# Kernel optimization log

Hardware: AMD Instinct MI355X
Metric: run time of the kernel (lower is better)

Reference implementation:

```python
import jax, jax.numpy as jnp
import numpy as np

B, T, XD, ZD, H = 1024, 1000, 8, 8, 256


def setup_inputs() -> dict:
    key = jax.random.key(0)
    ks = jax.random.split(key, 10)
    # monotonically increasing time grid, identical per batch element: [B, T, 1]
    t = jnp.broadcast_to(jnp.linspace(0.0, 10.0, T, dtype=jnp.float32)[None, :, None], (B, T, 1))
    x = jax.random.normal(ks[0], (B, T, XD), jnp.float32)
    z = jax.random.normal(ks[1], (B, T, ZD), jnp.float32)
    event_t = jax.random.uniform(ks[2], (B, 1), jnp.float32, 3.0, 7.0)
    z_jump = jax.random.normal(ks[3], (B, ZD), jnp.float32)
    in_dim = 3 * (XD + ZD)

    def lin(k, fan_in, fan_out):
        return jax.random.normal(k, (fan_in, fan_out), jnp.float32) * (1.0 / np.sqrt(fan_in))

    W1 = lin(ks[4], in_dim, H); b1 = jnp.zeros((H,), jnp.float32)
    W2 = lin(ks[5], H, H);     b2 = jnp.zeros((H,), jnp.float32)
    W3 = lin(ks[6], H, H);     b3 = jnp.zeros((H,), jnp.float32)
    W4 = lin(ks[7], H, XD);    b4 = jnp.zeros((XD,), jnp.float32)
    return dict(t=t, x=x, z=z, event_t=event_t, z_jump=z_jump,
                W1=W1, b1=b1, W2=W2, b2=b2, W3=W3, b3=b3, W4=W4, b4=b4)


def reference(t, x, z, event_t, z_jump, W1, b1, W2, b2, W3, b3, W4, b4):
    # all_initial = cat(x[:,0], z[:,0]) : [B, XD+ZD]
    all_initial = jnp.concatenate([x[:, 0], z[:, 0]], axis=-1)

    def de_func(x_cur, z_eff):
        xtzt = jnp.concatenate([x_cur, z_eff], axis=-1)                      # [B, XD+ZD]
        inp = jnp.concatenate([all_initial, xtzt - all_initial, xtzt], -1)   # [B, 3*(XD+ZD)]
        h = jax.nn.elu(inp @ W1 + b1)
        h = jax.nn.elu(h @ W2 + b2)
        h = jax.nn.elu(h @ W3 + b3)
        return h @ W4 + b4                                                   # [B, XD]

    t_seq = jnp.moveaxis(t, 1, 0)   # [T, B, 1]
    z_seq = jnp.moveaxis(z, 1, 0)   # [T, B, ZD]
    dt = t_seq[1:] - t_seq[:-1]     # [T-1, B, 1]

    def step(x_cur, step_in):
        t_i, dt_i, z_i = step_in
        # event: once t passes event_t, exogenous z jumps to z_jump
        z_eff = jnp.where(t_i >= event_t, z_jump, z_i)
        x_next = x_cur + dt_i * de_func(x_cur, z_eff)  # explicit Euler step
        return x_next, x_next

    x0 = x[:, 0]  # initial condition [B, XD]
    _, xs = jax.lax.scan(step, x0, (t_seq[:-1], dt, z_seq[:-1]))
    sol = jnp.concatenate([x0[None], xs], axis=0)  # [T, B, XD]
    return jnp.moveaxis(sol, 0, 1)                 # [B, T, XD]
```

## Files before the change

kernel.cpp:

```cpp
#include <hip/hip_runtime.h>
#include <cstdint>
#include <cstddef>

typedef __bf16 bf16x8 __attribute__((ext_vector_type(8)));
typedef float f32x4 __attribute__((ext_vector_type(4)));

#define HD 256
#define TLEN 1000
#define NSTEP 999

#define W1R_OFF 0
#define W2R_OFF 16384
#define W3R_OFF 81920
#define W4R_OFF 147456
#define WS_ELEMS 151552

__device__ __forceinline__ void wg_barrier() {
  asm volatile("s_waitcnt lgkmcnt(0)\n\ts_barrier" ::: "memory");
}

__global__ void prep_weights(const float* __restrict__ W1, const float* __restrict__ b1,
                             const float* __restrict__ W2, const float* __restrict__ W3,
                             const float* __restrict__ W4, __bf16* __restrict__ ws) {
  int tid = blockIdx.x * blockDim.x + threadIdx.x;
  if (tid >= WS_ELEMS) return;
  float val = 0.0f;
  if (tid < W2R_OFF) {
    int t = tid;
    int j = t & 7, lane = (t >> 3) & 63, tt = (t >> 9) & 1, kb = (t >> 10) & 1, w = (t >> 11) & 7;
    int k = kb * 32 + ((lane >> 4) * 8) + j;
    int n = w * 32 + tt * 16 + (lane & 15);
    if (k < 48) val = W1[k * HD + n];
    else if (k == 48) val = b1[n];
  } else if (tid < W3R_OFF) {
    int t = tid - W2R_OFF;
    int j = t & 7, lane = (t >> 3) & 63, tt = (t >> 9) & 1, kb = (t >> 10) & 7, w = (t >> 13) & 7;
    int k = kb * 32 + ((lane >> 4) * 8) + j;
    int n = w * 32 + tt * 16 + (lane & 15);
    val = W2[k * HD + n];
  } else if (tid < W4R_OFF) {
    int t = tid - W3R_OFF;
    int j = t & 7, lane = (t >> 3) & 63, tt = (t >> 9) & 1, kb = (t >> 10) & 7, w = (t >> 13) & 7;
    int k = kb * 32 + ((lane >> 4) * 8) + j;
    int n = w * 32 + tt * 16 + (lane & 15);
    val = W3[k * HD + n];
  } else {
    int t = tid - W4R_OFF;
    int j = t & 7, lane = (t >> 3) & 63, kb = (t >> 9) & 7;
    int k = kb * 32 + ((lane >> 4) * 8) + j;
    int n = lane & 15;
    val = (n < 8) ? W4[k * 8 + n] : 0.0f;
  }
  ws[tid] = (__bf16)val;
}

__global__ __launch_bounds__(512, 2) void ode_main(
    const float* __restrict__ t_g, const float* __restrict__ x_g,
    const float* __restrict__ z_g, const float* __restrict__ ev_g,
    const float* __restrict__ zj_g, const float* __restrict__ b2_g,
    const float* __restrict__ b3_g, const float* __restrict__ b4_g,
    const __bf16* __restrict__ ws, float* __restrict__ out) {
  __shared__ __align__(16) __bf16 h_a[16 * 264];
  __shared__ __align__(16) __bf16 h_b[16 * 264];
  __shared__ __align__(16) __bf16 w4sh[4096];
  __shared__ __align__(16) float x_cur[16 * 12];
  __shared__ __align__(16) float z_eff[16 * 12];
  __shared__ __align__(16) float x0s[16 * 12];
  __shared__ __align__(16) float z0s[16 * 12];
  __shared__ __align__(16) float zjs[16 * 12];
  __shared__ float evs[16];

  const int tid  = threadIdx.x;
  const int lane = tid & 63;
  const int wid  = tid >> 6;
  const int bcol = lane & 15;
  const int q    = lane >> 4;
  const int b0   = blockIdx.x * 16;

  if (tid < 128) {
    int m = tid >> 3, d = tid & 7;
    size_t gb = (size_t)(b0 + m);
    float x0 = x_g[gb * (TLEN * 8) + d];
    float z0 = z_g[gb * (TLEN * 8) + d];
    x0s[m * 12 + d] = x0;
    z0s[m * 12 + d] = z0;
    x_cur[m * 12 + d] = x0;
    zjs[m * 12 + d] = zj_g[gb * 8 + d];
    out[gb * (TLEN * 8) + d] = x0;
    if (d == 0) evs[m] = ev_g[gb];
  }
  {
    const uint32_t* s4 = (const uint32_t*)(ws + W4R_OFF);
    uint32_t* d4 = (uint32_t*)w4sh;
#pragma unroll
    for (int k = 0; k < 4; ++k) d4[tid * 4 + k] = s4[tid * 4 + k];
  }
  __syncthreads();

  if (tid < 128) {
    int m = tid >> 3, d = tid & 7;
    float t0 = t_g[0];
    z_eff[m * 12 + d] = (t0 >= evs[m]) ? zjs[m * 12 + d] : z0s[m * 12 + d];
  }

  const bf16x8* wsv = (const bf16x8*)ws;
  bf16x8 w1f[2][2], w2f[8][2], w3f[8][2];
#pragma unroll
  for (int kb = 0; kb < 2; ++kb)
#pragma unroll
    for (int tt = 0; tt < 2; ++tt)
      w1f[kb][tt] = wsv[(W1R_OFF / 8) + ((wid * 2 + kb) * 2 + tt) * 64 + lane];
#pragma unroll
  for (int kb = 0; kb < 8; ++kb)
#pragma unroll
    for (int tt = 0; tt < 2; ++tt) {
      w2f[kb][tt] = wsv[(W2R_OFF / 8) + ((wid * 8 + kb) * 2 + tt) * 64 + lane];
      w3f[kb][tt] = wsv[(W3R_OFF / 8) + ((wid * 8 + kb) * 2 + tt) * 64 + lane];
    }

  f32x4 b2v[2], b3v[2];
#pragma unroll
  for (int tt = 0; tt < 2; ++tt) {
    int n0 = wid * 32 + tt * 16 + q * 4;
    b2v[tt] = *(const f32x4*)(b2_g + n0);
    b3v[tt] = *(const f32x4*)(b3_g + n0);
  }
  f32x4 b4v = {0.f, 0.f, 0.f, 0.f};
  if (wid == 0 && q < 2) b4v = *(const f32x4*)(b4_g + q * 4);

  const int m1 = lane >> 2;
  const int d0 = (lane & 3) * 2;
  float2 zjf = make_float2(0.f, 0.f);
  float ev1 = 0.f;
  if (wid == 1) {
    zjf.x = zjs[m1 * 12 + d0];
    zjf.y = zjs[m1 * 12 + d0 + 1];
    ev1 = evs[m1];
  }

  f32x4 sub0, sub1;
  bf16x8 a0c;
  {
    const float* base = ((q & 1) ? z0s : x0s) + bcol * 12;
    f32x4 r0 = *(const f32x4*)(base);
    f32x4 r1 = *(const f32x4*)(base + 4);
    sub0 = r0; sub1 = r1;
#pragma unroll
    for (int e = 0; e < 4; ++e) { a0c[e] = (__bf16)r0[e]; a0c[e + 4] = (__bf16)r1[e]; }
  }
  bf16x8 zf;
#pragma unroll
  for (int e = 0; e < 8; ++e) zf[e] = (__bf16)0.f;
  bf16x8 k48f = zf;
  k48f[0] = (__bf16)1.0f;

  __syncthreads();

  float tc = t_g[0];

  auto layer = [&](const __bf16* src, __bf16* dst, const bf16x8 (*wf)[2], const f32x4* bv) {
    bf16x8 bfr[8];
    const bf16x8* hp = (const bf16x8*)src;
#pragma unroll
    for (int kb = 0; kb < 8; ++kb) bfr[kb] = hp[bcol * 33 + kb * 4 + q];
#pragma unroll
    for (int tt = 0; tt < 2; ++tt) {
      f32x4 c = bv[tt];
#pragma unroll
      for (int kb = 0; kb < 8; ++kb)
        c = __builtin_amdgcn_mfma_f32_16x16x32_bf16(wf[kb][tt], bfr[kb], c, 0, 0, 0);
      union { __bf16 h4[4]; unsigned long long u; } pk;
#pragma unroll
      for (int e = 0; e < 4; ++e) {
        float v = c[e];
        v = (v > 0.f) ? v : (__expf(v) - 1.0f);
        pk.h4[e] = (__bf16)v;
      }
      *(unsigned long long*)(dst + bcol * 264 + wid * 32 + tt * 16 + q * 4) = pk.u;
    }
  };

#pragma unroll 1
  for (int i = 0; i < NSTEP; ++i) {
    float tn = t_g[i + 1];
    float2 zpre = make_float2(0.f, 0.f);
    if (wid == 1)
      zpre = *(const float2*)(z_g + ((size_t)(b0 + m1) * TLEN + (i + 1)) * 8 + d0);

    {
      const float* rp = ((q & 1) ? z_eff : x_cur) + bcol * 12;
      f32x4 r0 = *(const f32x4*)(rp);
      f32x4 r1 = *(const f32x4*)(rp + 4);
      bf16x8 f0, f1;
      if (q < 2) {
        f0 = a0c;
#pragma unroll
        for (int e = 0; e < 4; ++e) { f1[e] = (__bf16)r0[e]; f1[e + 4] = (__bf16)r1[e]; }
      } else {
#pragma unroll
        for (int e = 0; e < 4; ++e) {
          f0[e] = (__bf16)(r0[e] - sub0[e]);
          f0[e + 4] = (__bf16)(r1[e] - sub1[e]);
        }
        f1 = (q == 2) ? k48f : zf;
      }
#pragma unroll
      for (int tt = 0; tt < 2; ++tt) {
        f32x4 c = {0.f, 0.f, 0.f, 0.f};
        c = __builtin_amdgcn_mfma_f32_16x16x32_bf16(w1f[0][tt], f0, c, 0, 0, 0);
        c = __builtin_amdgcn_mfma_f32_16x16x32_bf16(w1f[1][tt], f1, c, 0, 0, 0);
        union { __bf16 h4[4]; unsigned long long u; } pk;
#pragma unroll
        for (int e = 0; e < 4; ++e) {
          float v = c[e];
          v = (v > 0.f) ? v : (__expf(v) - 1.0f);
          pk.h4[e] = (__bf16)v;
        }
        *(unsigned long long*)(h_a + bcol * 264 + wid * 32 + tt * 16 + q * 4) = pk.u;
      }
    }
    wg_barrier();
    layer(h_a, h_b, w2f, b2v);
    wg_barrier();
    layer(h_b, h_a, w3f, b3v);
    wg_barrier();

    float dt = tn - tc;
    if (wid == 0) {
      const bf16x8* hp = (const bf16x8*)h_a;
      const bf16x8* w4p = (const bf16x8*)w4sh;
      f32x4 c = b4v;
#pragma unroll
      for (int kb = 0; kb < 8; ++kb)
        c = __builtin_amdgcn_mfma_f32_16x16x32_bf16(w4p[kb * 64 + lane],
                                                    hp[bcol * 33 + kb * 4 + q], c, 0, 0, 0);
      if (q < 2) {
        f32x4 xc = *(const f32x4*)(x_cur + bcol * 12 + q * 4);
        f32x4 xn;
#pragma unroll
        for (int e = 0; e < 4; ++e) xn[e] = xc[e] + dt * c[e];
        *(f32x4*)(x_cur + bcol * 12 + q * 4) = xn;
        *(f32x4*)(out + ((size_t)(b0 + bcol) * TLEN + (i + 1)) * 8 + q * 4) = xn;
      }
    } else if (wid == 1) {
      bool jmp = (tn >= ev1);
      float2 zev = make_float2(jmp ? zjf.x : zpre.x, jmp ? zjf.y : zpre.y);
      *(float2*)(z_eff + m1 * 12 + d0) = zev;
    }
    tc = tn;
    wg_barrier();
  }
}

extern "C" void kernel_launch(void* const* d_in, const int* in_sizes, int n_in,
                              void* d_out, int out_size, void* d_ws, size_t ws_size,
                              hipStream_t stream) {
  const float* t  = (const float*)d_in[0];
  const float* x  = (const float*)d_in[1];
  const float* z  = (const float*)d_in[2];
  const float* ev = (const float*)d_in[3];
  const float* zj = (const float*)d_in[4];
  const float* W1 = (const float*)d_in[5];
  const float* b1 = (const float*)d_in[6];
  const float* W2 = (const float*)d_in[7];
  const float* b2 = (const float*)d_in[8];
  const float* W3 = (const float*)d_in[9];
  const float* b3 = (const float*)d_in[10];
  const float* W4 = (const float*)d_in[11];
  const float* b4 = (const float*)d_in[12];
  __bf16* ws = (__bf16*)d_ws;
  float* out = (float*)d_out;

  prep_weights<<<592, 256, 0, stream>>>(W1, b1, W2, W3, W4, ws);
  ode_main<<<64, 512, 0, stream>>>(t, x, z, ev, zj, b2, b3, b4, ws, out);
}
```

Measured before the change: 1.833 ms.

## Halve workgroup to 4 waves and split final layer across all waves

Each workgroup now runs 4 waves instead of 8, and each wave holds weight fragments for 64 output columns instead of 32, so each wave issues twice the MFMAs per layer. The last layer, previously done by wave 0 alone from shared memory, is split across all four waves using register-resident W4 fragments. Their partial sums go through shared memory and are reduced by 128 threads before the Euler update. This cuts barrier participants and the serialized single-wave tail, at the cost of doubled register pressure per wave and fewer waves to hide latency.

```diff
diff --git a/kernel.cpp b/kernel.cpp
--- a/kernel.cpp
+++ b/kernel.cpp
@@ -54,7 +54,7 @@
   ws[tid] = (__bf16)val;
 }
 
-__global__ __launch_bounds__(512, 2) void ode_main(
+__global__ __launch_bounds__(256, 1) void ode_main(
     const float* __restrict__ t_g, const float* __restrict__ x_g,
     const float* __restrict__ z_g, const float* __restrict__ ev_g,
     const float* __restrict__ zj_g, const float* __restrict__ b2_g,
@@ -62,7 +62,7 @@
     const __bf16* __restrict__ ws, float* __restrict__ out) {
   __shared__ __align__(16) __bf16 h_a[16 * 264];
   __shared__ __align__(16) __bf16 h_b[16 * 264];
-  __shared__ __align__(16) __bf16 w4sh[4096];
+  __shared__ __align__(16) float p4[4 * 16 * 8];
   __shared__ __align__(16) float x_cur[16 * 12];
   __shared__ __align__(16) float z_eff[16 * 12];
   __shared__ __align__(16) float x0s[16 * 12];
@@ -89,12 +89,6 @@
     out[gb * (TLEN * 8) + d] = x0;
     if (d == 0) evs[m] = ev_g[gb];
   }
-  {
-    const uint32_t* s4 = (const uint32_t*)(ws + W4R_OFF);
-    uint32_t* d4 = (uint32_t*)w4sh;
-#pragma unroll
-    for (int k = 0; k < 4; ++k) d4[tid * 4 + k] = s4[tid * 4 + k];
-  }
   __syncthreads();
 
   if (tid < 128) {
@@ -104,35 +98,37 @@
   }
 
   const bf16x8* wsv = (const bf16x8*)ws;
-  bf16x8 w1f[2][2], w2f[8][2], w3f[8][2];
+  bf16x8 w1f[2][4], w2f[8][4], w3f[8][4];
 #pragma unroll
   for (int kb = 0; kb < 2; ++kb)
 #pragma unroll
-    for (int tt = 0; tt < 2; ++tt)
-      w1f[kb][tt] = wsv[(W1R_OFF / 8) + ((wid * 2 + kb) * 2 + tt) * 64 + lane];
+    for (int tt = 0; tt < 4; ++tt)
+      w1f[kb][tt] = wsv[(W1R_OFF / 8) + (((2 * wid + (tt >> 1)) * 2 + kb) * 2 + (tt & 1)) * 64 + lane];
 #pragma unroll
   for (int kb = 0; kb < 8; ++kb)
 #pragma unroll
-    for (int tt = 0; tt < 2; ++tt) {
-      w2f[kb][tt] = wsv[(W2R_OFF / 8) + ((wid * 8 + kb) * 2 + tt) * 64 + lane];
-      w3f[kb][tt] = wsv[(W3R_OFF / 8) + ((wid * 8 + kb) * 2 + tt) * 64 + lane];
-    }
-
-  f32x4 b2v[2], b3v[2];
-#pragma unroll
-  for (int tt = 0; tt < 2; ++tt) {
-    int n0 = wid * 32 + tt * 16 + q * 4;
+    for (int tt = 0; tt < 4; ++tt) {
+      int idx = (((2 * wid + (tt >> 1)) * 8 + kb) * 2 + (tt & 1)) * 64 + lane;
+      w2f[kb][tt] = wsv[(W2R_OFF / 8) + idx];
+      w3f[kb][tt] = wsv[(W3R_OFF / 8) + idx];
+    }
+  bf16x8 w4f0 = wsv[(W4R_OFF / 8) + (2 * wid) * 64 + lane];
+  bf16x8 w4f1 = wsv[(W4R_OFF / 8) + (2 * wid + 1) * 64 + lane];
+
+  f32x4 b2v[4], b3v[4];
+#pragma unroll
+  for (int tt = 0; tt < 4; ++tt) {
+    int n0 = wid * 64 + tt * 16 + q * 4;
     b2v[tt] = *(const f32x4*)(b2_g + n0);
     b3v[tt] = *(const f32x4*)(b3_g + n0);
   }
-  f32x4 b4v = {0.f, 0.f, 0.f, 0.f};
-  if (wid == 0 && q < 2) b4v = *(const f32x4*)(b4_g + q * 4);
+  float b4l = (tid < 128) ? b4_g[tid & 7] : 0.0f;
 
   const int m1 = lane >> 2;
   const int d0 = (lane & 3) * 2;
   float2 zjf = make_float2(0.f, 0.f);
   float ev1 = 0.f;
-  if (wid == 1) {
+  if (wid == 2) {
     zjf.x = zjs[m1 * 12 + d0];
     zjf.y = zjs[m1 * 12 + d0 + 1];
     ev1 = evs[m1];
@@ -158,13 +154,13 @@
 
   float tc = t_g[0];
 
-  auto layer = [&](const __bf16* src, __bf16* dst, const bf16x8 (*wf)[2], const f32x4* bv) {
+  auto layer_full = [&](const __bf16* src, __bf16* dst, const bf16x8 (*wf)[4], const f32x4* bv) {
     bf16x8 bfr[8];
     const bf16x8* hp = (const bf16x8*)src;
 #pragma unroll
     for (int kb = 0; kb < 8; ++kb) bfr[kb] = hp[bcol * 33 + kb * 4 + q];
 #pragma unroll
-    for (int tt = 0; tt < 2; ++tt) {
+    for (int tt = 0; tt < 4; ++tt) {
       f32x4 c = bv[tt];
 #pragma unroll
       for (int kb = 0; kb < 8; ++kb)
@@ -176,7 +172,7 @@
         v = (v > 0.f) ? v : (__expf(v) - 1.0f);
         pk.h4[e] = (__bf16)v;
       }
-      *(unsigned long long*)(dst + bcol * 264 + wid * 32 + tt * 16 + q * 4) = pk.u;
+      *(unsigned long long*)(dst + bcol * 264 + wid * 64 + tt * 16 + q * 4) = pk.u;
     }
   };
 
@@ -184,7 +180,7 @@
   for (int i = 0; i < NSTEP; ++i) {
     float tn = t_g[i + 1];
     float2 zpre = make_float2(0.f, 0.f);
-    if (wid == 1)
+    if (wid == 2)
       zpre = *(const float2*)(z_g + ((size_t)(b0 + m1) * TLEN + (i + 1)) * 8 + d0);
 
     {
@@ -205,7 +201,7 @@
         f1 = (q == 2) ? k48f : zf;
       }
 #pragma unroll
-      for (int tt = 0; tt < 2; ++tt) {
+      for (int tt = 0; tt < 4; ++tt) {
         f32x4 c = {0.f, 0.f, 0.f, 0.f};
         c = __builtin_amdgcn_mfma_f32_16x16x32_bf16(w1f[0][tt], f0, c, 0, 0, 0);
         c = __builtin_amdgcn_mfma_f32_16x16x32_bf16(w1f[1][tt], f1, c, 0, 0, 0);
@@ -216,33 +212,36 @@
           v = (v > 0.f) ? v : (__expf(v) - 1.0f);
           pk.h4[e] = (__bf16)v;
         }
-        *(unsigned long long*)(h_a + bcol * 264 + wid * 32 + tt * 16 + q * 4) = pk.u;
+        *(unsigned long long*)(h_a + bcol * 264 + wid * 64 + tt * 16 + q * 4) = pk.u;
       }
     }
     wg_barrier();
-    layer(h_a, h_b, w2f, b2v);
-    wg_barrier();
-    layer(h_b, h_a, w3f, b3v);
+    layer_full(h_a, h_b, w2f, b2v);
+    wg_barrier();
+    layer_full(h_b, h_a, w3f, b3v);
+
+    {
+      const bf16x8* hp = (const bf16x8*)h_a;
+      bf16x8 h40 = hp[bcol * 33 + (2 * wid) * 4 + q];
+      bf16x8 h41 = hp[bcol * 33 + (2 * wid + 1) * 4 + q];
+      f32x4 c = {0.f, 0.f, 0.f, 0.f};
+      c = __builtin_amdgcn_mfma_f32_16x16x32_bf16(w4f0, h40, c, 0, 0, 0);
+      c = __builtin_amdgcn_mfma_f32_16x16x32_bf16(w4f1, h41, c, 0, 0, 0);
+      if (q < 2)
+        *(f32x4*)(p4 + wid * 128 + bcol * 8 + q * 4) = c;
+    }
     wg_barrier();
 
     float dt = tn - tc;
-    if (wid == 0) {
-      const bf16x8* hp = (const bf16x8*)h_a;
-      const bf16x8* w4p = (const bf16x8*)w4sh;
-      f32x4 c = b4v;
-#pragma unroll
-      for (int kb = 0; kb < 8; ++kb)
-        c = __builtin_amdgcn_mfma_f32_16x16x32_bf16(w4p[kb * 64 + lane],
-                                                    hp[bcol * 33 + kb * 4 + q], c, 0, 0, 0);
-      if (q < 2) {
-        f32x4 xc = *(const f32x4*)(x_cur + bcol * 12 + q * 4);
-        f32x4 xn;
-#pragma unroll
-        for (int e = 0; e < 4; ++e) xn[e] = xc[e] + dt * c[e];
-        *(f32x4*)(x_cur + bcol * 12 + q * 4) = xn;
-        *(f32x4*)(out + ((size_t)(b0 + bcol) * TLEN + (i + 1)) * 8 + q * 4) = xn;
-      }
-    } else if (wid == 1) {
+    if (tid < 128) {
+      int m = tid >> 3, d = tid & 7;
+      float s = b4l;
+#pragma unroll
+      for (int j = 0; j < 4; ++j) s += p4[j * 128 + m * 8 + d];
+      float xn = x_cur[m * 12 + d] + dt * s;
+      x_cur[m * 12 + d] = xn;
+      out[(size_t)(b0 + m) * (TLEN * 8) + (size_t)(i + 1) * 8 + d] = xn;
+    } else if (wid == 2) {
       bool jmp = (tn >= ev1);
       float2 zev = make_float2(jmp ? zjf.x : zpre.x, jmp ? zjf.y : zpre.y);
       *(float2*)(z_eff + m1 * 12 + d0) = zev;
@@ -272,5 +271,5 @@
   float* out = (float*)d_out;
 
   prep_weights<<<592, 256, 0, stream>>>(W1, b1, W2, W3, W4, ws);
-  ode_main<<<64, 512, 0, stream>>>(t, x, z, ev, zj, b2, b3, b4, ws, out);
-}
+  ode_main<<<64, 256, 0, stream>>>(t, x, z, ev, zj, b2, b3, b4, ws, out);
+}
```

After: 2.295 ms. 1.25x slower.
